# Optimization experiments

Measured on AMD Instinct MI355X. Metric: run time of the kernel, lower is better.

## Reference

```python
import jax, jax.numpy as jnp
import numpy as np

B, S, E, H, D = 4, 2048, 1024, 16, 64


def setup_inputs() -> dict:
    key = jax.random.key(0)
    ks = jax.random.split(key, 10)
    s_in = 1.0 / np.sqrt(E)
    s_out = 1.0 / np.sqrt(H * D)
    return {
        "x": jax.random.normal(ks[0], (B, S, E), dtype=jnp.float32),
        "wq": jax.random.uniform(ks[1], (H, E, D), jnp.float32, -s_in, s_in),
        "bq": jax.random.uniform(ks[2], (H, D), jnp.float32, -s_in, s_in),
        "wk": jax.random.uniform(ks[3], (H, E, D), jnp.float32, -s_in, s_in),
        "bk": jax.random.uniform(ks[4], (H, D), jnp.float32, -s_in, s_in),
        "wv": jax.random.uniform(ks[5], (H, E, D), jnp.float32, -s_in, s_in),
        "bv": jax.random.uniform(ks[6], (H, D), jnp.float32, -s_in, s_in),
        "wo": jax.random.uniform(ks[7], (H * D, E), jnp.float32, -s_out, s_out),
        "bo": jax.random.uniform(ks[8], (E,), jnp.float32, -s_out, s_out),
    }


def reference(x, wq, bq, wk, bk, wv, bv, wo, bo):
    # Batched equivalent of the per-head Python loop: project all heads at once.
    q = jnp.einsum("bse,hed->bhsd", x, wq) + bq[None, :, None, :]
    k = jnp.einsum("bse,hed->bhsd", x, wk) + bk[None, :, None, :]
    v = jnp.einsum("bse,hed->bhsd", x, wv) + bv[None, :, None, :]
    scale = 1.0 / jnp.sqrt(jnp.asarray(D, dtype=x.dtype))
    scores = jnp.einsum("bhsd,bhtd->bhst", q, k) * scale  # [B,H,S,S]
    causal = jnp.tril(jnp.ones((S, S), dtype=bool))
    scores = jnp.where(causal[None, None], scores, jnp.asarray(-jnp.inf, x.dtype))
    p = jax.nn.softmax(scores, axis=-1)
    o = jnp.einsum("bhst,bhtd->bhsd", p, v)
    # concat heads along last dim (head order matches the torch cat order)
    o = jnp.transpose(o, (0, 2, 1, 3)).reshape(B, S, H * D)
    y = o @ wo + bo  # output projection; dropout is identity in eval
    return y
```

## Files before the change

kernel.cpp:

```cpp
#include <hip/hip_runtime.h>
#include <math.h>

#define B_ 4
#define S_ 2048
#define E_ 1024
#define H_ 16
#define D_ 64

using f32x4 = __attribute__((ext_vector_type(4))) float;
using s16x8 = __attribute__((ext_vector_type(8))) short;

__device__ __forceinline__ unsigned short f2bf(float f) {
    unsigned int u = __float_as_uint(f);
    u = (u + 0x7FFFu + ((u >> 16) & 1u)) >> 16;
    return (unsigned short)u;
}

__device__ __forceinline__ unsigned int cvt_pk_bf16(float lo, float hi) {
    unsigned int r;
    asm("v_cvt_pk_bf16_f32 %0, %1, %2" : "=v"(r) : "v"(lo), "v"(hi));
    return r;
}

__device__ __forceinline__ float fast_exp2(float x) {
#if __has_builtin(__builtin_amdgcn_exp2f)
    return __builtin_amdgcn_exp2f(x);
#else
    return exp2f(x);
#endif
}

__device__ __forceinline__ void load_lds16(const void* g, void* l) {
    __builtin_amdgcn_global_load_lds(
        (const __attribute__((address_space(1))) void*)g,
        (__attribute__((address_space(3))) void*)l, 16, 0, 0);
}

#define WAITV(n) asm volatile("s_waitcnt vmcnt(" #n ")" ::: "memory")
#define WAITL(n) asm volatile("s_waitcnt lgkmcnt(" #n ")" ::: "memory")
#define SCHEDB __builtin_amdgcn_sched_barrier(0)

#define QSCALE 0.18033688011112042f

__global__ __launch_bounds__(256)
void cast_x(const float* __restrict__ in, unsigned short* __restrict__ out)
{
    const size_t idx = (size_t)blockIdx.x * 2048 + threadIdx.x * 8;
    const float4 v0 = *(const float4*)&in[idx];
    const float4 v1 = *(const float4*)&in[idx + 4];
    uint4 p;
    p.x = (unsigned)f2bf(v0.x) | ((unsigned)f2bf(v0.y) << 16);
    p.y = (unsigned)f2bf(v0.z) | ((unsigned)f2bf(v0.w) << 16);
    p.z = (unsigned)f2bf(v1.x) | ((unsigned)f2bf(v1.y) << 16);
    p.w = (unsigned)f2bf(v1.z) | ((unsigned)f2bf(v1.w) << 16);
    *(uint4*)&out[idx] = p;
}

__global__ __launch_bounds__(256)
void transpose_w(const float* __restrict__ wq, const float* __restrict__ wk,
                 const float* __restrict__ wv, const float* __restrict__ wo,
                 unsigned short* __restrict__ Wqkvt, unsigned short* __restrict__ Wot)
{
    __shared__ float T[64][68];
    const int z = blockIdx.z;
    const float* in;
    unsigned short* out;
    int inStride, r0, c0;
    if (z < 48) {
        if (blockIdx.y != 0) return;
        const int t = z >> 4, h = z & 15;
        const float* W = (t == 0) ? wq : ((t == 1) ? wk : wv);
        in = W + (size_t)h * (E_ * D_);
        inStride = 64;
        out = Wqkvt + (size_t)(t * 1024 + h * 64) * 1024;
        r0 = blockIdx.x * 64; c0 = 0;
    } else {
        in = wo; inStride = 1024;
        out = Wot;
        r0 = blockIdx.x * 64; c0 = blockIdx.y * 64;
    }
    const int tid = threadIdx.x;
    #pragma unroll
    for (int i = 0; i < 4; ++i) {
        const int e = tid + i * 256;
        const int row = e >> 4, c4 = e & 15;
        const float4 v = *(const float4*)&in[(size_t)(r0 + row) * inStride + c0 + c4 * 4];
        T[row][c4 * 4 + 0] = v.x; T[row][c4 * 4 + 1] = v.y;
        T[row][c4 * 4 + 2] = v.z; T[row][c4 * 4 + 3] = v.w;
    }
    __syncthreads();
    #pragma unroll
    for (int i = 0; i < 2; ++i) {
        const int e = tid + i * 256;
        const int c = e >> 3, ch = e & 7;
        unsigned short h8[8];
        #pragma unroll
        for (int j = 0; j < 8; ++j) h8[j] = f2bf(T[ch * 8 + j][c]);
        uint4 p;
        p.x = (unsigned)h8[0] | ((unsigned)h8[1] << 16);
        p.y = (unsigned)h8[2] | ((unsigned)h8[3] << 16);
        p.z = (unsigned)h8[4] | ((unsigned)h8[5] << 16);
        p.w = (unsigned)h8[6] | ((unsigned)h8[7] << 16);
        *(uint4*)&out[(size_t)(c0 + c) * 1024 + r0 + ch * 8] = p;
    }
}

template<int MODE>
__global__ __launch_bounds__(512, 2)
void gemm_mfma(const unsigned short* __restrict__ A,
               const unsigned short* __restrict__ Bt,
               const float* __restrict__ bq, const float* __restrict__ bk,
               const float* __restrict__ bv, const float* __restrict__ bo,
               unsigned short* __restrict__ Qb, unsigned short* __restrict__ Kb,
               unsigned short* __restrict__ Vt, float* __restrict__ Cout)
{
    __shared__ short As[3][128 * 64];
    __shared__ short Bs[3][256 * 64];

    const int tid  = threadIdx.x;
    const int w    = tid >> 6, lane = tid & 63;
    const int g    = lane >> 4, l15 = lane & 15;
    const int wm   = w >> 2, wn = w & 3;
    const int mbase = blockIdx.x * 128;
    const int nbase = blockIdx.y * 256;

    const int srow   = lane >> 3;
    const int schunk = (lane & 7) ^ srow;
    const size_t aoff = (size_t)(mbase + srow) * 1024 + schunk * 8;
    const size_t boff = (size_t)(nbase + srow) * 1024 + schunk * 8;

    f32x4 acc[4][4];
    #pragma unroll
    for (int mt = 0; mt < 4; ++mt)
        #pragma unroll
        for (int nt = 0; nt < 4; ++nt)
            acc[mt][nt] = (f32x4){0.f, 0.f, 0.f, 0.f};

    auto STAGE = [&](int t, int buf) {
        #pragma unroll
        for (int i = 0; i < 2; ++i) {
            const int u = w * 2 + i;
            load_lds16(&A[aoff + (size_t)(u * 8) * 1024 + t * 64], &As[buf][u * 512]);
        }
        #pragma unroll
        for (int i = 0; i < 4; ++i) {
            const int u = w * 4 + i;
            load_lds16(&Bt[boff + (size_t)(u * 8) * 1024 + t * 64], &Bs[buf][u * 512]);
        }
    };

    const int pr  = l15 & 7;
    const int pc0 = (g ^ pr) * 8;
    const int pc1 = ((4 + g) ^ pr) * 8;

    s16x8 a0[4], b0[4], a1[4], b1[4];
    auto LDF = [&](s16x8* af, s16x8* bf, int buf, int pc) {
        #pragma unroll
        for (int mt = 0; mt < 4; ++mt)
            af[mt] = *(const s16x8*)&As[buf][(wm * 64 + mt * 16 + l15) * 64 + pc];
        #pragma unroll
        for (int nt = 0; nt < 4; ++nt)
            bf[nt] = *(const s16x8*)&Bs[buf][(wn * 64 + nt * 16 + l15) * 64 + pc];
    };
    auto MFMA16 = [&](const s16x8* af, const s16x8* bf) {
        __builtin_amdgcn_s_setprio(1);
        #pragma unroll
        for (int mt = 0; mt < 4; ++mt)
            #pragma unroll
            for (int nt = 0; nt < 4; ++nt)
                acc[mt][nt] = __builtin_amdgcn_mfma_f32_16x16x32_bf16(
                    af[mt], bf[nt], acc[mt][nt], 0, 0, 0);
        __builtin_amdgcn_s_setprio(0);
    };

    STAGE(0, 0); STAGE(1, 1);
    WAITV(6);
    __builtin_amdgcn_s_barrier();
    LDF(a0, b0, 0, pc0);

    #pragma unroll 1
    for (int t = 0; t < 16; ++t) {
        const int buf = t % 3;
        LDF(a1, b1, buf, pc1);
        if (t + 2 < 16) STAGE(t + 2, (t + 2) % 3);
        WAITL(8); SCHEDB;
        MFMA16(a0, b0);
        WAITL(0); SCHEDB;
        if (t < 15) {
            if (t < 14) { WAITV(6); } else { WAITV(0); }
            __builtin_amdgcn_s_barrier();
            LDF(a0, b0, (t + 1) % 3, pc0);
            WAITL(8); SCHEDB;
        }
        MFMA16(a1, b1);
    }

    #pragma unroll
    for (int nt = 0; nt < 4; ++nt) {
        const int ncol = nbase + wn * 64 + nt * 16 + l15;
        if (MODE == 0) {
            const int tt = ncol >> 10;
            const int hh = (ncol >> 6) & 15;
            const int d  = ncol & 63;
            const float* bias = (tt == 0) ? bq : ((tt == 1) ? bk : bv);
            const float sc = (tt == 0) ? QSCALE : 1.0f;
            const float bval = bias[hh * 64 + d];
            #pragma unroll
            for (int mt = 0; mt < 4; ++mt)
                #pragma unroll
                for (int r = 0; r < 4; ++r) {
                    const int m = mbase + wm * 64 + mt * 16 + g * 4 + r;
                    const int b = m >> 11, s = m & 2047;
                    const unsigned short val = f2bf((acc[mt][nt][r] + bval) * sc);
                    if (tt == 2)
                        Vt[((size_t)(b * 16 + hh) * 64 + d) * 2048 + s] = val;
                    else {
                        unsigned short* Out = (tt == 0) ? Qb : Kb;
                        Out[((size_t)(b * 16 + hh) * 2048 + s) * 64 + d] = val;
                    }
                }
        } else {
            const float bval = bo[ncol];
            #pragma unroll
            for (int mt = 0; mt < 4; ++mt)
                #pragma unroll
                for (int r = 0; r < 4; ++r) {
                    const int m = mbase + wm * 64 + mt * 16 + g * 4 + r;
                    Cout[(size_t)m * 1024 + ncol] = acc[mt][nt][r] + bval;
                }
        }
    }
}

#define LDK 72
__global__ __launch_bounds__(512, 2)
void attn_mfma(const unsigned short* __restrict__ Qb,
               const unsigned short* __restrict__ Kb,
               const unsigned short* __restrict__ Vt,
               unsigned short* __restrict__ O)
{
    __shared__ short Kls[2][64 * LDK];
    __shared__ short Vls[2][64 * LDK];
    __shared__ short Pls[8][16 * LDK];

    const int tid  = threadIdx.x;
    const int w    = tid >> 6;
    const int lane = tid & 63;
    const int g    = lane >> 4;
    const int l15  = lane & 15;
    const int j    = blockIdx.x;
    const int j2   = 15 - j;
    const int h    = blockIdx.y;
    const int b    = blockIdx.z;

    const size_t hb = (size_t)(b * 16 + h) * (2048 * 64);
    const int qH = j2 * 128 + w * 16;
    const int qL = j * 128 + w * 16;

    s16x8 aqH[2], aqL[2];
    {
        const int rh = qH + l15, rl = qL + l15;
        aqH[0] = *(const s16x8*)&Qb[hb + (size_t)rh * 64 + g * 8];
        aqH[1] = *(const s16x8*)&Qb[hb + (size_t)rh * 64 + 32 + g * 8];
        aqL[0] = *(const s16x8*)&Qb[hb + (size_t)rl * 64 + g * 8];
        aqL[1] = *(const s16x8*)&Qb[hb + (size_t)rl * 64 + 32 + g * 8];
    }

    const s16x8 ones = (s16x8){(short)0x3F80, (short)0x3F80, (short)0x3F80,
                               (short)0x3F80, (short)0x3F80, (short)0x3F80,
                               (short)0x3F80, (short)0x3F80};

    f32x4 lsumHa = (f32x4){0.f,0.f,0.f,0.f};
    f32x4 lsumLa = (f32x4){0.f,0.f,0.f,0.f};
    f32x4 OH[4], OL[4];
    #pragma unroll
    for (int nt = 0; nt < 4; ++nt) { OH[nt] = (f32x4){0.f,0.f,0.f,0.f}; OL[nt] = (f32x4){0.f,0.f,0.f,0.f}; }

    const int stages      = 32 - 2 * j;
    const int lightStages = 2 * j + 2;

    const int srow = tid >> 3, spart = tid & 7;
    uint4 kreg = *(const uint4*)&Kb[hb + (size_t)srow * 64 + spart * 8];
    uint4 vreg = *(const uint4*)&Vt[hb + (size_t)srow * 2048 + spart * 8];

    for (int t = 0; t < stages; ++t) {
        const int t0  = t * 64;
        const int buf = t & 1;
        *(uint4*)&Kls[buf][srow * LDK + spart * 8] = kreg;
        *(uint4*)&Vls[buf][srow * LDK + spart * 8] = vreg;
        if (t + 1 < stages) {
            kreg = *(const uint4*)&Kb[hb + (size_t)(t0 + 64 + srow) * 64 + spart * 8];
            vreg = *(const uint4*)&Vt[hb + (size_t)srow * 2048 + t0 + 64 + spart * 8];
        }
        __syncthreads();

        #pragma unroll
        for (int half = 0; half < 2; ++half) {
            if (half == 1 && t >= lightStages) break;
            const s16x8* aq   = (half == 0) ? aqH : aqL;
            const int qbase   = (half == 0) ? qH : qL;
            f32x4* Oacc       = (half == 0) ? OH : OL;
            f32x4* lsa        = (half == 0) ? &lsumHa : &lsumLa;

            f32x4 Sf[4];
            #pragma unroll
            for (int ct = 0; ct < 4; ++ct) {
                f32x4 acc = (f32x4){0.f, 0.f, 0.f, 0.f};
                const s16x8 bk0 = *(const s16x8*)&Kls[buf][(ct * 16 + l15) * LDK + g * 8];
                const s16x8 bk1 = *(const s16x8*)&Kls[buf][(ct * 16 + l15) * LDK + 32 + g * 8];
                acc = __builtin_amdgcn_mfma_f32_16x16x32_bf16(bk0, aq[0], acc, 0, 0, 0);
                acc = __builtin_amdgcn_mfma_f32_16x16x32_bf16(bk1, aq[1], acc, 0, 0, 0);
                Sf[ct] = acc;
            }

            if (t0 + 63 > qbase) {
                const int query = qbase + l15;
                #pragma unroll
                for (int ct = 0; ct < 4; ++ct) {
                    const int kbase = t0 + ct * 16 + g * 4;
                    #pragma unroll
                    for (int r = 0; r < 4; ++r)
                        if (kbase + r > query) Sf[ct][r] = -1e30f;
                }
            }

            #pragma unroll
            for (int ct = 0; ct < 4; ++ct)
                #pragma unroll
                for (int r = 0; r < 4; ++r) Sf[ct][r] = fast_exp2(Sf[ct][r]);

            #pragma unroll
            for (int ct = 0; ct < 4; ++ct) {
                uint2 pw;
                pw.x = cvt_pk_bf16(Sf[ct][0], Sf[ct][1]);
                pw.y = cvt_pk_bf16(Sf[ct][2], Sf[ct][3]);
                *(uint2*)&Pls[w][l15 * LDK + ct * 16 + g * 4] = pw;
            }

            const s16x8 pf0 = *(const s16x8*)&Pls[w][l15 * LDK + g * 8];
            const s16x8 pf1 = *(const s16x8*)&Pls[w][l15 * LDK + 32 + g * 8];
            *lsa = __builtin_amdgcn_mfma_f32_16x16x32_bf16(ones, pf0, *lsa, 0, 0, 0);
            *lsa = __builtin_amdgcn_mfma_f32_16x16x32_bf16(ones, pf1, *lsa, 0, 0, 0);
            #pragma unroll
            for (int nt = 0; nt < 4; ++nt) {
                const s16x8 bv0 = *(const s16x8*)&Vls[buf][(nt * 16 + l15) * LDK + g * 8];
                const s16x8 bv1 = *(const s16x8*)&Vls[buf][(nt * 16 + l15) * LDK + 32 + g * 8];
                Oacc[nt] = __builtin_amdgcn_mfma_f32_16x16x32_bf16(bv0, pf0, Oacc[nt], 0, 0, 0);
                Oacc[nt] = __builtin_amdgcn_mfma_f32_16x16x32_bf16(bv1, pf1, Oacc[nt], 0, 0, 0);
            }
        }
    }

    const float invH = 1.0f / lsumHa[0];
    const float invL = 1.0f / lsumLa[0];

    #pragma unroll
    for (int half = 0; half < 2; ++half) {
        const f32x4* Oacc = (half == 0) ? OH : OL;
        const float  inv  = (half == 0) ? invH : invL;
        const int query   = ((half == 0) ? qH : qL) + l15;
        #pragma unroll
        for (int nt = 0; nt < 4; ++nt) {
            uint2 pk;
            pk.x = cvt_pk_bf16(Oacc[nt][0] * inv, Oacc[nt][1] * inv);
            pk.y = cvt_pk_bf16(Oacc[nt][2] * inv, Oacc[nt][3] * inv);
            *(uint2*)&O[(size_t)(b * 2048 + query) * 1024 + h * 64 + nt * 16 + g * 4] = pk;
        }
    }
}

extern "C" void kernel_launch(void* const* d_in, const int* in_sizes, int n_in,
                              void* d_out, int out_size, void* d_ws, size_t ws_size,
                              hipStream_t stream) {
    const float* x  = (const float*)d_in[0];
    const float* wq = (const float*)d_in[1];
    const float* bq = (const float*)d_in[2];
    const float* wk = (const float*)d_in[3];
    const float* bk = (const float*)d_in[4];
    const float* wv = (const float*)d_in[5];
    const float* bv = (const float*)d_in[6];
    const float* wo = (const float*)d_in[7];
    const float* bo = (const float*)d_in[8];
    float* out = (float*)d_out;

    const size_t hsz = (size_t)B_ * H_ * S_ * D_;
    unsigned short* xb    = (unsigned short*)d_ws;
    unsigned short* Wqkvt = xb + hsz;
    unsigned short* Wot   = Wqkvt + (size_t)3072 * 1024;
    unsigned short* Qb    = Wot + (size_t)1024 * 1024;
    unsigned short* Kb    = Qb + hsz;
    unsigned short* Vt    = Kb + hsz;
    unsigned short* Ob    = Vt + hsz;

    cast_x<<<4096, 256, 0, stream>>>(x, xb);
    transpose_w<<<dim3(16, 16, 49), 256, 0, stream>>>(wq, wk, wv, wo, Wqkvt, Wot);
    gemm_mfma<0><<<dim3(64, 12), 512, 0, stream>>>(
        xb, Wqkvt, bq, bk, bv, nullptr, Qb, Kb, Vt, nullptr);
    attn_mfma<<<dim3(8, H_, B_), 512, 0, stream>>>(Qb, Kb, Vt, Ob);
    gemm_mfma<1><<<dim3(64, 4), 512, 0, stream>>>(
        Ob, Wot, nullptr, nullptr, nullptr, bo, nullptr, nullptr, nullptr, out);
}
```

Baseline: 258.7 us.

## Retile projection GEMMs to 256-row blocks with phased double-buffered staging

```diff
diff --git a/kernel.cpp b/kernel.cpp
--- a/kernel.cpp
+++ b/kernel.cpp
@@ -114,38 +114,46 @@
                unsigned short* __restrict__ Qb, unsigned short* __restrict__ Kb,
                unsigned short* __restrict__ Vt, float* __restrict__ Cout)
 {
-    __shared__ short As[3][128 * 64];
-    __shared__ short Bs[3][256 * 64];
+    constexpr int BN  = (MODE == 0) ? 192 : 128;
+    constexpr int NTF = BN / 64;
+
+    __shared__ short As[2][256 * 64];
+    __shared__ short Bs[2][BN * 64];
 
     const int tid  = threadIdx.x;
     const int w    = tid >> 6, lane = tid & 63;
     const int g    = lane >> 4, l15 = lane & 15;
     const int wm   = w >> 2, wn = w & 3;
-    const int mbase = blockIdx.x * 128;
-    const int nbase = blockIdx.y * 256;
+    const int mbase = blockIdx.x * 256;
+    const int nbase = blockIdx.y * BN;
 
     const int srow   = lane >> 3;
     const int schunk = (lane & 7) ^ srow;
     const size_t aoff = (size_t)(mbase + srow) * 1024 + schunk * 8;
     const size_t boff = (size_t)(nbase + srow) * 1024 + schunk * 8;
 
-    f32x4 acc[4][4];
-    #pragma unroll
-    for (int mt = 0; mt < 4; ++mt)
-        #pragma unroll
-        for (int nt = 0; nt < 4; ++nt)
+    f32x4 acc[8][NTF];
+    #pragma unroll
+    for (int mt = 0; mt < 8; ++mt)
+        #pragma unroll
+        for (int nt = 0; nt < NTF; ++nt)
             acc[mt][nt] = (f32x4){0.f, 0.f, 0.f, 0.f};
 
-    auto STAGE = [&](int t, int buf) {
+    auto STAGE_B = [&](int t, int buf) {
+        #pragma unroll
+        for (int i = 0; i < NTF; ++i) {
+            const int u = w * NTF + i;
+            load_lds16(&Bt[boff + (size_t)(u * 8) * 1024 + t * 64],
+                       &Bs[buf][u * 512]);
+        }
+    };
+    auto STAGE_A = [&](int t, int buf, int qm) {
         #pragma unroll
         for (int i = 0; i < 2; ++i) {
-            const int u = w * 2 + i;
-            load_lds16(&A[aoff + (size_t)(u * 8) * 1024 + t * 64], &As[buf][u * 512]);
-        }
-        #pragma unroll
-        for (int i = 0; i < 4; ++i) {
-            const int u = w * 4 + i;
-            load_lds16(&Bt[boff + (size_t)(u * 8) * 1024 + t * 64], &Bs[buf][u * 512]);
+            const int idx = w * 2 + i;
+            const int u   = idx + (idx & 8) + qm * 8;
+            load_lds16(&A[aoff + (size_t)(u * 8) * 1024 + t * 64],
+                       &As[buf][u * 512]);
         }
     };
 
@@ -153,51 +161,69 @@
     const int pc0 = (g ^ pr) * 8;
     const int pc1 = ((4 + g) ^ pr) * 8;
 
-    s16x8 a0[4], b0[4], a1[4], b1[4];
-    auto LDF = [&](s16x8* af, s16x8* bf, int buf, int pc) {
-        #pragma unroll
-        for (int mt = 0; mt < 4; ++mt)
-            af[mt] = *(const s16x8*)&As[buf][(wm * 64 + mt * 16 + l15) * 64 + pc];
-        #pragma unroll
-        for (int nt = 0; nt < 4; ++nt)
-            bf[nt] = *(const s16x8*)&Bs[buf][(wn * 64 + nt * 16 + l15) * 64 + pc];
+    s16x8 af[4], bf[NTF];
+    auto LDA = [&](int buf, int qm, int pc) {
+        #pragma unroll
+        for (int i = 0; i < 4; ++i)
+            af[i] = *(const s16x8*)&As[buf][(wm * 128 + (qm * 4 + i) * 16 + l15) * 64 + pc];
     };
-    auto MFMA16 = [&](const s16x8* af, const s16x8* bf) {
+    auto LDB = [&](int buf, int pc) {
+        #pragma unroll
+        for (int nt = 0; nt < NTF; ++nt)
+            bf[nt] = *(const s16x8*)&Bs[buf][(wn * (NTF * 16) + nt * 16 + l15) * 64 + pc];
+    };
+    auto MFMA_PH = [&](int qm) {
         __builtin_amdgcn_s_setprio(1);
         #pragma unroll
-        for (int mt = 0; mt < 4; ++mt)
-            #pragma unroll
-            for (int nt = 0; nt < 4; ++nt)
-                acc[mt][nt] = __builtin_amdgcn_mfma_f32_16x16x32_bf16(
-                    af[mt], bf[nt], acc[mt][nt], 0, 0, 0);
+        for (int i = 0; i < 4; ++i)
+            #pragma unroll
+            for (int nt = 0; nt < NTF; ++nt)
+                acc[qm * 4 + i][nt] = __builtin_amdgcn_mfma_f32_16x16x32_bf16(
+                    af[i], bf[nt], acc[qm * 4 + i][nt], 0, 0, 0);
         __builtin_amdgcn_s_setprio(0);
     };
 
-    STAGE(0, 0); STAGE(1, 1);
-    WAITV(6);
+    STAGE_B(0, 0); STAGE_A(0, 0, 0); STAGE_A(0, 0, 1);
+    WAITV(2);
     __builtin_amdgcn_s_barrier();
-    LDF(a0, b0, 0, pc0);
 
     #pragma unroll 1
     for (int t = 0; t < 16; ++t) {
-        const int buf = t % 3;
-        LDF(a1, b1, buf, pc1);
-        if (t + 2 < 16) STAGE(t + 2, (t + 2) % 3);
-        WAITL(8); SCHEDB;
-        MFMA16(a0, b0);
+        const int buf = t & 1, nbuf = buf ^ 1;
+
+        LDA(buf, 0, pc0); LDB(buf, pc0);
+        if (t < 15) {
+            STAGE_B(t + 1, nbuf);
+            if constexpr (MODE == 0) { WAITV(3); } else { WAITV(2); }
+        } else {
+            WAITV(0);
+        }
+        __builtin_amdgcn_s_barrier();
         WAITL(0); SCHEDB;
-        if (t < 15) {
-            if (t < 14) { WAITV(6); } else { WAITV(0); }
-            __builtin_amdgcn_s_barrier();
-            LDF(a0, b0, (t + 1) % 3, pc0);
-            WAITL(8); SCHEDB;
-        }
-        MFMA16(a1, b1);
-    }
-
-    #pragma unroll
-    for (int nt = 0; nt < 4; ++nt) {
-        const int ncol = nbase + wn * 64 + nt * 16 + l15;
+        MFMA_PH(0);
+
+        LDA(buf, 1, pc0);
+        if (t < 15) STAGE_A(t + 1, nbuf, 0);
+        __builtin_amdgcn_s_barrier();
+        WAITL(0); SCHEDB;
+        MFMA_PH(1);
+
+        LDA(buf, 0, pc1); LDB(buf, pc1);
+        if (t < 15) STAGE_A(t + 1, nbuf, 1);
+        __builtin_amdgcn_s_barrier();
+        WAITL(0); SCHEDB;
+        MFMA_PH(0);
+
+        LDA(buf, 1, pc1);
+        if (t < 15) { WAITV(2); }
+        __builtin_amdgcn_s_barrier();
+        WAITL(0); SCHEDB;
+        MFMA_PH(1);
+    }
+
+    #pragma unroll
+    for (int nt = 0; nt < NTF; ++nt) {
+        const int ncol = nbase + wn * (NTF * 16) + nt * 16 + l15;
         if (MODE == 0) {
             const int tt = ncol >> 10;
             const int hh = (ncol >> 6) & 15;
@@ -206,10 +232,10 @@
             const float sc = (tt == 0) ? QSCALE : 1.0f;
             const float bval = bias[hh * 64 + d];
             #pragma unroll
-            for (int mt = 0; mt < 4; ++mt)
+            for (int mt = 0; mt < 8; ++mt)
                 #pragma unroll
                 for (int r = 0; r < 4; ++r) {
-                    const int m = mbase + wm * 64 + mt * 16 + g * 4 + r;
+                    const int m = mbase + wm * 128 + mt * 16 + g * 4 + r;
                     const int b = m >> 11, s = m & 2047;
                     const unsigned short val = f2bf((acc[mt][nt][r] + bval) * sc);
                     if (tt == 2)
@@ -222,10 +248,10 @@
         } else {
             const float bval = bo[ncol];
             #pragma unroll
-            for (int mt = 0; mt < 4; ++mt)
+            for (int mt = 0; mt < 8; ++mt)
                 #pragma unroll
                 for (int r = 0; r < 4; ++r) {
-                    const int m = mbase + wm * 64 + mt * 16 + g * 4 + r;
+                    const int m = mbase + wm * 128 + mt * 16 + g * 4 + r;
                     Cout[(size_t)m * 1024 + ncol] = acc[mt][nt][r] + bval;
                 }
         }
@@ -394,9 +420,9 @@
 
     cast_x<<<4096, 256, 0, stream>>>(x, xb);
     transpose_w<<<dim3(16, 16, 49), 256, 0, stream>>>(wq, wk, wv, wo, Wqkvt, Wot);
-    gemm_mfma<0><<<dim3(64, 12), 512, 0, stream>>>(
+    gemm_mfma<0><<<dim3(32, 16), 512, 0, stream>>>(
         xb, Wqkvt, bq, bk, bv, nullptr, Qb, Kb, Vt, nullptr);
     attn_mfma<<<dim3(8, H_, B_), 512, 0, stream>>>(Qb, Kb, Vt, Ob);
-    gemm_mfma<1><<<dim3(64, 4), 512, 0, stream>>>(
+    gemm_mfma<1><<<dim3(32, 8), 512, 0, stream>>>(
         Ob, Wot, nullptr, nullptr, nullptr, bo, nullptr, nullptr, nullptr, out);
 }
```

Measured after the change: 275.4 us. 1.06x slower.
